# Kernel optimization log

Measured on AMD Instinct MI355X. Metric: run time of the kernel, lower is better.

Reference implementation:

```python
import jax, jax.numpy as jnp
import numpy as np

N, E, F_IN, H, C, P, E2, B, NCLS = 150000, 1500000, 64, 64, 50000, 300000, 600000, 16, 10
EPS = 1e-5


def setup_inputs() -> dict:
    key = jax.random.key(0)
    ks = jax.random.split(key, 20)
    f32 = jnp.float32

    def lin_w(k, i, o):
        return jax.random.normal(k, (i, o), f32) / np.float32(np.sqrt(i))

    return {
        "x": jax.random.normal(ks[0], (N, F_IN), f32),
        "edge_index": jax.random.randint(ks[1], (2, E), 0, N),
        "weights": jax.random.uniform(ks[2], (E,), f32),
        "batch": jnp.sort(jax.random.randint(ks[3], (N,), 0, B)),
        "cover_n": jax.random.randint(ks[4], (P,), 0, N),
        "cover_c": jax.random.randint(ks[5], (P,), 0, C),
        "edge_index2": jax.random.randint(ks[6], (2, E2), 0, C),
        "weights2": jax.random.uniform(ks[7], (E2,), f32),
        "batch2": jnp.sort(jax.random.randint(ks[8], (C,), 0, B)),
        "W_in0": lin_w(ks[9], F_IN, H), "b_in0": jnp.zeros((H,), f32),
        "W_in1": lin_w(ks[10], H, H), "b_in1": jnp.zeros((H,), f32),
        "Wl_in": lin_w(ks[11], 2 * H, H), "bl_in": jnp.zeros((H,), f32),
        "W_b0": lin_w(ks[12], 2 * H, H), "b_b0": jnp.zeros((H,), f32),
        "W_b1": lin_w(ks[13], H, H), "b_b1": jnp.zeros((H,), f32),
        "Wl_b": lin_w(ks[14], 2 * H, H), "bl_b": jnp.zeros((H,), f32),
        "bn_gamma": jnp.ones((4 * H,), f32), "bn_beta": jnp.zeros((4 * H,), f32),
        "lin1_W": lin_w(ks[15], 4 * H, H), "lin1_b": jnp.zeros((H,), f32),
        "lin2_W": lin_w(ks[16], H, NCLS), "lin2_b": jnp.zeros((NCLS,), f32),
    }


def _gcn(x, row, col, ew, W, b, n):
    # GCNConv with edge weights: sym-normalized adjacency, messages flow row->col
    h = x @ W
    deg = jax.ops.segment_sum(ew, col, num_segments=n)
    dis = jnp.where(deg > 0, jax.lax.rsqrt(deg), 0.0)
    norm = dis[row] * ew * dis[col]  # [E']
    return jax.ops.segment_sum(norm[:, None] * h[row], col, num_segments=n) + b


def _block(x, edge_index, ew, n, W0, b0, W1, b1, Wl, bl):
    # Block(num_layers=2, mode='cat'): two GCN+relu, JK-cat, Linear
    loop = jnp.arange(n)
    row = jnp.concatenate([edge_index[0], loop])  # add self loops (w=1)
    col = jnp.concatenate([edge_index[1], loop])
    ew = jnp.concatenate([ew, jnp.ones((n,), ew.dtype)])
    x1 = jax.nn.relu(_gcn(x, row, col, ew, W0, b0, n))
    x2 = jax.nn.relu(_gcn(x1, row, col, ew, W1, b1, n))
    return jnp.concatenate([x1, x2], axis=1) @ Wl + bl


def _segmax0(x, ids, n):
    m = jax.ops.segment_max(x, ids, num_segments=n)
    return jnp.where(jnp.isfinite(m), m, 0.0)  # empty segments -> 0


def reference(x, edge_index, weights, batch, cover_n, cover_c, edge_index2,
              weights2, batch2, W_in0, b_in0, W_in1, b_in1, Wl_in, bl_in,
              W_b0, b_b0, W_b1, b_b1, Wl_b, bl_b, bn_gamma, bn_beta,
              lin1_W, lin1_b, lin2_W, lin2_b):
    # conv_in on the original graph
    x1 = jax.nn.relu(_block(x, edge_index, weights, N,
                            W_in0, b_in0, W_in1, b_in1, Wl_in, bl_in))
    xs = [jax.ops.segment_sum(x1, batch, num_segments=B), _segmax0(x1, batch, B)]
    # cover-index scatter pooling: add + max over clusters
    xg = x1[cover_n]  # [P, H]
    xp = jnp.concatenate([
        jax.ops.segment_sum(xg, cover_c, num_segments=C),
        _segmax0(xg, cover_c, C),
    ], axis=1)  # [C, 2H]
    # block on the pooled graph
    x2 = jax.nn.relu(_block(xp, edge_index2, weights2, C,
                            W_b0, b_b0, W_b1, b_b1, Wl_b, bl_b))
    xs += [jax.ops.segment_sum(x2, batch2, num_segments=B), _segmax0(x2, batch2, B)]
    h = jnp.concatenate(xs, axis=1)  # [B, 4H]
    mu = h.mean(axis=0)
    var = ((h - mu) ** 2).mean(axis=0)
    h = (h - mu) * jax.lax.rsqrt(var + EPS) * bn_gamma + bn_beta
    h = jax.nn.relu(h @ lin1_W + lin1_b)
    return jax.nn.softmax(h @ lin2_W + lin2_b, axis=-1)
```

## Files before the change

### kernel.cpp

```cpp
#include <hip/hip_runtime.h>

#define N_NODES 150000
#define E_EDGES 1500000
#define C_CLUST 50000
#define P_PAIRS 300000
#define E2_EDGES 600000
#define B_BATCH 16
#define EPS_ 1e-5f

static __device__ __forceinline__ void atomicMaxFloatPos(float* addr, float v) {
    atomicMax((int*)addr, __float_as_int(v));
}


__global__ void cnt_ids_kernel(const int* __restrict__ ids, int* __restrict__ cnt, int P) {
    int p = blockIdx.x * blockDim.x + threadIdx.x;
    if (p < P) atomicAdd(&cnt[ids[p]], 1);
}

__global__ __launch_bounds__(256) void scan1_kernel(const int* __restrict__ cnt,
                                                    int* __restrict__ exc,
                                                    int* __restrict__ bsum, int n) {
    __shared__ int sh[256];
    int t = threadIdx.x;
    int base = blockIdx.x * 1024 + t * 4;
    int v[4];
    #pragma unroll
    for (int i = 0; i < 4; ++i) { int idx = base + i; v[i] = (idx < n) ? cnt[idx] : 0; }
    int tsum = v[0] + v[1] + v[2] + v[3];
    sh[t] = tsum; __syncthreads();
    for (int o = 1; o < 256; o <<= 1) {
        int add = (t >= o) ? sh[t - o] : 0;
        __syncthreads();
        sh[t] += add;
        __syncthreads();
    }
    int run = sh[t] - tsum;
    #pragma unroll
    for (int i = 0; i < 4; ++i) { int idx = base + i; if (idx < n) exc[idx] = run; run += v[i]; }
    if (t == 255) bsum[blockIdx.x] = sh[255];
}

__global__ __launch_bounds__(256) void scan2_kernel(int* __restrict__ bsum, int nb,
                                                    int* __restrict__ total_out) {
    __shared__ int sh[256];
    int t = threadIdx.x;
    int val = (t < nb) ? bsum[t] : 0;
    sh[t] = val; __syncthreads();
    for (int o = 1; o < 256; o <<= 1) {
        int add = (t >= o) ? sh[t - o] : 0;
        __syncthreads();
        sh[t] += add;
        __syncthreads();
    }
    if (t < nb) bsum[t] = sh[t] - val;
    if (t == nb - 1) *total_out = sh[t];
}

__global__ void scan3_kernel(const int* __restrict__ exc, const int* __restrict__ bsum,
                             int* __restrict__ rowptr, int* __restrict__ next, int n) {
    int i = blockIdx.x * blockDim.x + threadIdx.x;
    if (i < n) {
        int v = exc[i] + bsum[i >> 10];
        rowptr[i] = v;
        next[i] = v;
    }
}


__global__ void bucket_kernel(const int* __restrict__ ei, const float* __restrict__ ew,
                              int* __restrict__ next, int* __restrict__ src,
                              float* __restrict__ ewc, int E) {
    int e = blockIdx.x * blockDim.x + threadIdx.x;
    if (e >= E) return;
    int r = ei[e], c = ei[E + e];
    int pos = atomicAdd(&next[c], 1);
    src[pos] = r;
    ewc[pos] = ew[e];
}

__global__ void bucketP_kernel(const int* __restrict__ cn, const int* __restrict__ cc,
                               int* __restrict__ next, int* __restrict__ srcn, int P) {
    int p = blockIdx.x * blockDim.x + threadIdx.x;
    if (p >= P) return;
    int pos = atomicAdd(&next[cc[p]], 1);
    srcn[pos] = cn[p];
}


__global__ void dis_csr_kernel(const int* __restrict__ rowptr, const float* __restrict__ ewc,
                               float* __restrict__ dis, int n) {
    int c = blockIdx.x * blockDim.x + threadIdx.x;
    if (c >= n) return;
    int j0 = rowptr[c], j1 = rowptr[c + 1];
    float s = 0.f;
    for (int j = j0; j < j1; ++j) s += ewc[j];
    dis[c] = rsqrtf(s + 1.0f);
}


__global__ void nw_csr_kernel(const int* __restrict__ rowptr, const int* __restrict__ src,
                              float* __restrict__ ewc, const float* __restrict__ dis, int n) {
    int c = blockIdx.x * blockDim.x + threadIdx.x;
    if (c >= n) return;
    float dc = dis[c];
    int j0 = rowptr[c], j1 = rowptr[c + 1];
    for (int j = j0; j < j1; ++j)
        ewc[j] = dis[src[j]] * ewc[j] * dc;
}


__global__ void gcn_gather_kernel(const float* __restrict__ h, const int* __restrict__ rowptr,
                                  const int* __restrict__ src, const float* __restrict__ nw,
                                  const float* __restrict__ dis, const float* __restrict__ bias,
                                  float* __restrict__ out, int n) {
    int t = blockIdx.x * blockDim.x + threadIdx.x;
    int c = t >> 6, lane = t & 63;
    if (c >= n) return;
    float d = dis[c];
    float acc = bias[lane] + d * d * h[(size_t)c * 64 + lane];
    int j = rowptr[c], e1 = rowptr[c + 1];
    for (; j + 3 < e1; j += 4) {
        int   r0 = src[j],  r1 = src[j + 1], r2 = src[j + 2], r3 = src[j + 3];
        float w0 = nw[j],   w1 = nw[j + 1],  w2 = nw[j + 2],  w3 = nw[j + 3];
        float h0 = h[(size_t)r0 * 64 + lane];
        float h1 = h[(size_t)r1 * 64 + lane];
        float h2 = h[(size_t)r2 * 64 + lane];
        float h3 = h[(size_t)r3 * 64 + lane];
        acc += w0 * h0; acc += w1 * h1; acc += w2 * h2; acc += w3 * h3;
    }
    for (; j < e1; ++j) acc += nw[j] * h[(size_t)src[j] * 64 + lane];
    out[(size_t)c * 64 + lane] = acc;
}

__global__ void cover_gather_kernel(const float* __restrict__ X, const int* __restrict__ rowptr,
                                    const int* __restrict__ srcn, float* __restrict__ xp_sum,
                                    float* __restrict__ xp_max, int C) {
    int t = blockIdx.x * blockDim.x + threadIdx.x;
    int c = t >> 6, lane = t & 63;
    if (c >= C) return;
    float s = 0.f, m = 0.f;
    int j = rowptr[c], e1 = rowptr[c + 1];
    for (; j + 1 < e1; j += 2) {
        float v0 = X[(size_t)srcn[j] * 64 + lane];
        float v1 = X[(size_t)srcn[j + 1] * 64 + lane];
        s += v0 + v1; m = fmaxf(m, fmaxf(v0, v1));
    }
    if (j < e1) {
        float v = X[(size_t)srcn[j] * 64 + lane];
        s += v; m = fmaxf(m, v);
    }
    xp_sum[(size_t)c * 64 + lane] = s;
    xp_max[(size_t)c * 64 + lane] = m;
}


template<int K, bool RELU_IN, bool RELU_OUT, bool HAS_X2, bool HAS_BIAS>
__global__ __launch_bounds__(256) void gemm_kernel(const float* __restrict__ X1,
                                                   const float* __restrict__ X2,
                                                   const float* __restrict__ W,
                                                   const float* __restrict__ bias,
                                                   float* __restrict__ Y, int n) {
    constexpr int KP = K + 4;
    __shared__ float Xs[64 * KP];
    __shared__ float Ws[K * 64];
    const int tid = threadIdx.x;
    const int r0 = blockIdx.x * 64;

    for (int i = tid; i < K * 16; i += 256)
        ((float4*)Ws)[i] = ((const float4*)W)[i];

    for (int i = tid; i < 16 * K; i += 256) {
        int row = i / (K / 4);
        int k4  = (i % (K / 4)) * 4;
        int r = r0 + row;
        float4 v = make_float4(0.f, 0.f, 0.f, 0.f);
        if (r < n) {
            const float* s = (HAS_X2 && k4 >= 64) ? (X2 + (size_t)r * 64 + (k4 - 64))
                                                  : (X1 + (size_t)r * 64 + k4);
            v = *(const float4*)s;
            if (RELU_IN) {
                v.x = fmaxf(v.x, 0.f); v.y = fmaxf(v.y, 0.f);
                v.z = fmaxf(v.z, 0.f); v.w = fmaxf(v.w, 0.f);
            }
        }
        *(float4*)&Xs[row * KP + k4] = v;
    }
    __syncthreads();

    const int tx = tid & 15, ty = tid >> 4;
    const int c0 = tx * 4, rl = ty * 4;
    float acc[4][4] = {};

    for (int k = 0; k < K; k += 4) {
        float4 xv[4], wv[4];
        #pragma unroll
        for (int i = 0; i < 4; ++i) xv[i] = *(const float4*)&Xs[(rl + i) * KP + k];
        #pragma unroll
        for (int i = 0; i < 4; ++i) wv[i] = *(const float4*)&Ws[(k + i) * 64 + c0];
        #pragma unroll
        for (int i = 0; i < 4; ++i) {
            const float* xp = (const float*)&xv[i];
            #pragma unroll
            for (int kk = 0; kk < 4; ++kk) {
                const float* wp = (const float*)&wv[kk];
                #pragma unroll
                for (int j = 0; j < 4; ++j) acc[i][j] += xp[kk] * wp[j];
            }
        }
    }

    #pragma unroll
    for (int i = 0; i < 4; ++i) {
        int r = r0 + rl + i;
        if (r < n) {
            float o[4];
            #pragma unroll
            for (int j = 0; j < 4; ++j) {
                o[j] = acc[i][j];
                if (HAS_BIAS) o[j] += bias[c0 + j];
                if (RELU_OUT) o[j] = fmaxf(o[j], 0.f);
            }
            *(float4*)&Y[(size_t)r * 64 + c0] = make_float4(o[0], o[1], o[2], o[3]);
        }
    }
}


__global__ void batch_pool_kernel(const float* __restrict__ X, const int* __restrict__ batch,
                                  int n, float* __restrict__ xs, int col_off, int rows_per_block) {
    int lane = threadIdx.x;
    int rstart = blockIdx.x * rows_per_block;
    if (rstart >= n) return;
    int rend = min(rstart + rows_per_block, n);
    float s = 0.f, m = 0.f;
    int cur = batch[rstart];
    for (int r = rstart; r < rend; ++r) {
        int b = batch[r];
        if (b != cur) {
            atomicAdd(&xs[cur * 256 + col_off + lane], s);
            atomicMaxFloatPos(&xs[cur * 256 + col_off + 64 + lane], m);
            s = 0.f; m = 0.f; cur = b;
        }
        float v = X[(size_t)r * 64 + lane];
        s += v; m = fmaxf(m, v);
    }
    atomicAdd(&xs[cur * 256 + col_off + lane], s);
    atomicMaxFloatPos(&xs[cur * 256 + col_off + 64 + lane], m);
}


__global__ __launch_bounds__(256) void head_kernel(const float* __restrict__ xs,
    const float* __restrict__ gamma, const float* __restrict__ beta,
    const float* __restrict__ W1, const float* __restrict__ b1,
    const float* __restrict__ W2, const float* __restrict__ b2,
    float* __restrict__ out) {
    __shared__ float hn[16][256];
    __shared__ float h2[16][64];
    __shared__ float logits[16][10];
    int t = threadIdx.x;

    float v[16];
    float mu = 0.f;
    #pragma unroll
    for (int b = 0; b < 16; ++b) { v[b] = xs[b * 256 + t]; mu += v[b]; }
    mu *= (1.f / 16.f);
    float var = 0.f;
    #pragma unroll
    for (int b = 0; b < 16; ++b) { float d = v[b] - mu; var += d * d; }
    var *= (1.f / 16.f);
    float sc = rsqrtf(var + EPS_) * gamma[t];
    float bt = beta[t];
    #pragma unroll
    for (int b = 0; b < 16; ++b) hn[b][t] = (v[b] - mu) * sc + bt;
    __syncthreads();

    {
        int c = t & 63, bg = t >> 6;
        for (int j = 0; j < 4; ++j) {
            int b = bg * 4 + j;
            float acc = b1[c];
            for (int k = 0; k < 256; ++k) acc += hn[b][k] * W1[k * 64 + c];
            h2[b][c] = fmaxf(acc, 0.f);
        }
    }
    __syncthreads();

    if (t < 160) {
        int b = t / 10, c = t % 10;
        float acc = b2[c];
        for (int k = 0; k < 64; ++k) acc += h2[b][k] * W2[k * 10 + c];
        logits[b][c] = acc;
    }
    __syncthreads();

    if (t < 16) {
        float m = -1e30f;
        for (int c = 0; c < 10; ++c) m = fmaxf(m, logits[t][c]);
        float s = 0.f;
        float e[10];
        for (int c = 0; c < 10; ++c) { e[c] = expf(logits[t][c] - m); s += e[c]; }
        float inv = 1.f / s;
        for (int c = 0; c < 10; ++c) out[t * 10 + c] = e[c] * inv;
    }
}

extern "C" void kernel_launch(void* const* d_in, const int* in_sizes, int n_in,
                              void* d_out, int out_size, void* d_ws, size_t ws_size,
                              hipStream_t stream) {
    (void)in_sizes; (void)n_in; (void)out_size; (void)ws_size;
    const float* x      = (const float*)d_in[0];
    const int*   ei1    = (const int*)d_in[1];
    const float* w1     = (const float*)d_in[2];
    const int*   batch  = (const int*)d_in[3];
    const int*   covern = (const int*)d_in[4];
    const int*   coverc = (const int*)d_in[5];
    const int*   ei2    = (const int*)d_in[6];
    const float* w2     = (const float*)d_in[7];
    const int*   batch2 = (const int*)d_in[8];
    const float* W_in0  = (const float*)d_in[9];
    const float* b_in0  = (const float*)d_in[10];
    const float* W_in1  = (const float*)d_in[11];
    const float* b_in1  = (const float*)d_in[12];
    const float* Wl_in  = (const float*)d_in[13];
    const float* bl_in  = (const float*)d_in[14];
    const float* W_b0   = (const float*)d_in[15];
    const float* b_b0   = (const float*)d_in[16];
    const float* W_b1   = (const float*)d_in[17];
    const float* b_b1   = (const float*)d_in[18];
    const float* Wl_b   = (const float*)d_in[19];
    const float* bl_b   = (const float*)d_in[20];
    const float* gamma  = (const float*)d_in[21];
    const float* beta   = (const float*)d_in[22];
    const float* lin1W  = (const float*)d_in[23];
    const float* lin1b  = (const float*)d_in[24];
    const float* lin2W  = (const float*)d_in[25];
    const float* lin2b  = (const float*)d_in[26];
    float* out = (float*)d_out;

    char* ws = (char*)d_ws;
    size_t off = 0;
    auto alloc = [&](size_t bytes) {
        char* p = ws + off; off += (bytes + 255) & ~(size_t)255; return p;
    };
    float* A   = (float*)alloc((size_t)N_NODES * 64 * 4);
    float* Bb  = (float*)alloc((size_t)N_NODES * 64 * 4);
    float* Cc  = (float*)alloc((size_t)N_NODES * 64 * 4);
    float* D   = (float*)alloc((size_t)N_NODES * 4);
    float* XS  = (float*)alloc((size_t)B_BATCH * 256 * 4);
    int*   bsum = (int*)alloc(256 * 4);
    char*  csr  = alloc(14 * 1024 * 1024);

    int*   cnt1    = (int*)csr;
    int*   next1   = cnt1 + N_NODES;
    int*   rowptr1 = next1 + N_NODES;
    int*   src1    = rowptr1 + (N_NODES + 1);
    float* nw1     = (float*)(src1 + E_EDGES);
    int*   cnt2    = (int*)csr;
    int*   next2   = cnt2 + C_CLUST;
    int*   rowptr2 = next2 + C_CLUST;
    int*   src2    = rowptr2 + (C_CLUST + 1);
    float* nw2     = (float*)(src2 + E2_EDGES);
    int*   cntP    = (int*)(nw2 + E2_EDGES);
    int*   nextP   = cntP + C_CLUST;
    int*   rowptrP = nextP + C_CLUST;
    int*   srcP    = rowptrP + (C_CLUST + 1);

    float* A2     = A  + (size_t)C_CLUST * 64;
    float* xp_sum = Bb;
    float* xp_max = Bb + (size_t)C_CLUST * 64;

    auto cdiv = [](long long a, long long b) { return (int)((a + b - 1) / b); };

    hipMemsetAsync(XS, 0, B_BATCH * 256 * 4, stream);

    hipMemsetAsync(cnt1, 0, N_NODES * 4, stream);
    cnt_ids_kernel<<<cdiv(E_EDGES, 256), 256, 0, stream>>>(ei1 + E_EDGES, cnt1, E_EDGES);
    scan1_kernel<<<cdiv(N_NODES, 1024), 256, 0, stream>>>(cnt1, next1, bsum, N_NODES);
    scan2_kernel<<<1, 256, 0, stream>>>(bsum, cdiv(N_NODES, 1024), rowptr1 + N_NODES);
    scan3_kernel<<<cdiv(N_NODES, 256), 256, 0, stream>>>(next1, bsum, rowptr1, next1, N_NODES);
    bucket_kernel<<<cdiv(E_EDGES, 256), 256, 0, stream>>>(ei1, w1, next1, src1, nw1, E_EDGES);
    dis_csr_kernel<<<cdiv(N_NODES, 256), 256, 0, stream>>>(rowptr1, nw1, D, N_NODES);
    nw_csr_kernel<<<cdiv(N_NODES, 256), 256, 0, stream>>>(rowptr1, src1, nw1, D, N_NODES);

    gemm_kernel<64, false, false, false, false><<<cdiv(N_NODES, 64), 256, 0, stream>>>(
        x, nullptr, W_in0, nullptr, A, N_NODES);
    gcn_gather_kernel<<<cdiv((long long)N_NODES * 64, 256), 256, 0, stream>>>(
        A, rowptr1, src1, nw1, D, b_in0, Bb, N_NODES);
    gemm_kernel<64, true, false, false, false><<<cdiv(N_NODES, 64), 256, 0, stream>>>(
        Bb, nullptr, W_in1, nullptr, A, N_NODES);
    gcn_gather_kernel<<<cdiv((long long)N_NODES * 64, 256), 256, 0, stream>>>(
        A, rowptr1, src1, nw1, D, b_in1, Cc, N_NODES);
    gemm_kernel<128, true, true, true, true><<<cdiv(N_NODES, 64), 256, 0, stream>>>(
        Bb, Cc, Wl_in, bl_in, A, N_NODES);

    batch_pool_kernel<<<cdiv(N_NODES, 64), 64, 0, stream>>>(A, batch, N_NODES, XS, 0, 64);

    hipMemsetAsync(cntP, 0, C_CLUST * 4, stream);
    cnt_ids_kernel<<<cdiv(P_PAIRS, 256), 256, 0, stream>>>(coverc, cntP, P_PAIRS);
    scan1_kernel<<<cdiv(C_CLUST, 1024), 256, 0, stream>>>(cntP, nextP, bsum, C_CLUST);
    scan2_kernel<<<1, 256, 0, stream>>>(bsum, cdiv(C_CLUST, 1024), rowptrP + C_CLUST);
    scan3_kernel<<<cdiv(C_CLUST, 256), 256, 0, stream>>>(nextP, bsum, rowptrP, nextP, C_CLUST);
    bucketP_kernel<<<cdiv(P_PAIRS, 256), 256, 0, stream>>>(covern, coverc, nextP, srcP, P_PAIRS);
    cover_gather_kernel<<<cdiv((long long)C_CLUST * 64, 256), 256, 0, stream>>>(
        A, rowptrP, srcP, xp_sum, xp_max, C_CLUST);

    hipMemsetAsync(cnt2, 0, C_CLUST * 4, stream);
    cnt_ids_kernel<<<cdiv(E2_EDGES, 256), 256, 0, stream>>>(ei2 + E2_EDGES, cnt2, E2_EDGES);
    scan1_kernel<<<cdiv(C_CLUST, 1024), 256, 0, stream>>>(cnt2, next2, bsum, C_CLUST);
    scan2_kernel<<<1, 256, 0, stream>>>(bsum, cdiv(C_CLUST, 1024), rowptr2 + C_CLUST);
    scan3_kernel<<<cdiv(C_CLUST, 256), 256, 0, stream>>>(next2, bsum, rowptr2, next2, C_CLUST);
    bucket_kernel<<<cdiv(E2_EDGES, 256), 256, 0, stream>>>(ei2, w2, next2, src2, nw2, E2_EDGES);
    dis_csr_kernel<<<cdiv(C_CLUST, 256), 256, 0, stream>>>(rowptr2, nw2, D, C_CLUST);
    nw_csr_kernel<<<cdiv(C_CLUST, 256), 256, 0, stream>>>(rowptr2, src2, nw2, D, C_CLUST);

    gemm_kernel<128, false, false, true, false><<<cdiv(C_CLUST, 64), 256, 0, stream>>>(
        xp_sum, xp_max, W_b0, nullptr, Cc, C_CLUST);
    gcn_gather_kernel<<<cdiv((long long)C_CLUST * 64, 256), 256, 0, stream>>>(
        Cc, rowptr2, src2, nw2, D, b_b0, A, C_CLUST);
    gemm_kernel<64, true, false, false, false><<<cdiv(C_CLUST, 64), 256, 0, stream>>>(
        A, nullptr, W_b1, nullptr, Cc, C_CLUST);
    gcn_gather_kernel<<<cdiv((long long)C_CLUST * 64, 256), 256, 0, stream>>>(
        Cc, rowptr2, src2, nw2, D, b_b1, A2, C_CLUST);
    gemm_kernel<128, true, true, true, true><<<cdiv(C_CLUST, 64), 256, 0, stream>>>(
        A, A2, Wl_b, bl_b, Cc, C_CLUST);

    batch_pool_kernel<<<cdiv(C_CLUST, 64), 64, 0, stream>>>(Cc, batch2, C_CLUST, XS, 128, 64);

    head_kernel<<<1, 256, 0, stream>>>(XS, gamma, beta, lin1W, lin1b, lin2W, lin2b, out);
}
```

Baseline: 927.7 us.

## Fuse GCN gather with following dense linear layers via wave shuffles

Replaces the separate gather, gemm, gather and JK-concat gemm kernels with a fused kernel. Each wavefront aggregates neighbours for a node and immediately multiplies the relu'd result by a weight matrix staged in shared memory, using lane shuffles. This removes intermediate activation round-trips through global memory and several launches. The cost is a per-node 64- or 128-step shuffle matvec and a weight reload into shared memory for every block of 16 nodes.

```diff
diff --git a/kernel.cpp b/kernel.cpp
--- a/kernel.cpp
+++ b/kernel.cpp
@@ -109,28 +109,60 @@
         ewc[j] = dis[src[j]] * ewc[j] * dc;
 }
 
-
-__global__ void gcn_gather_kernel(const float* __restrict__ h, const int* __restrict__ rowptr,
-                                  const int* __restrict__ src, const float* __restrict__ nw,
-                                  const float* __restrict__ dis, const float* __restrict__ bias,
-                                  float* __restrict__ out, int n) {
-    int t = blockIdx.x * blockDim.x + threadIdx.x;
-    int c = t >> 6, lane = t & 63;
-    if (c >= n) return;
-    float d = dis[c];
-    float acc = bias[lane] + d * d * h[(size_t)c * 64 + lane];
-    int j = rowptr[c], e1 = rowptr[c + 1];
-    for (; j + 3 < e1; j += 4) {
-        int   r0 = src[j],  r1 = src[j + 1], r2 = src[j + 2], r3 = src[j + 3];
-        float w0 = nw[j],   w1 = nw[j + 1],  w2 = nw[j + 2],  w3 = nw[j + 3];
-        float h0 = h[(size_t)r0 * 64 + lane];
-        float h1 = h[(size_t)r1 * 64 + lane];
-        float h2 = h[(size_t)r2 * 64 + lane];
-        float h3 = h[(size_t)r3 * 64 + lane];
-        acc += w0 * h0; acc += w1 * h1; acc += w2 * h2; acc += w3 * h3;
-    }
-    for (; j < e1; ++j) acc += nw[j] * h[(size_t)src[j] * 64 + lane];
-    out[(size_t)c * 64 + lane] = acc;
+template<bool HAS_PRE>
+__global__ __launch_bounds__(256) void fused_gather_gemm_kernel(
+    const float* __restrict__ h, const int* __restrict__ rowptr,
+    const int* __restrict__ src, const float* __restrict__ nw,
+    const float* __restrict__ dis, const float* __restrict__ bias_g,
+    const float* __restrict__ pre, const float* __restrict__ W,
+    const float* __restrict__ bias2, float* __restrict__ agg_out,
+    float* __restrict__ out, int n) {
+    constexpr int KW = HAS_PRE ? 128 : 64;
+    __shared__ float Ws[KW * 64];
+    const int tid = threadIdx.x;
+    for (int i = tid; i < KW * 16; i += 256)
+        ((float4*)Ws)[i] = ((const float4*)W)[i];
+    __syncthreads();
+
+    const int lane = tid & 63, wid = tid >> 6;
+    const int c0 = blockIdx.x * 16 + wid * 4;
+    for (int i = 0; i < 4; ++i) {
+        int c = c0 + i;
+        if (c >= n) break;
+        float d = dis[c];
+        float acc = bias_g[lane] + d * d * h[(size_t)c * 64 + lane];
+        int j = rowptr[c], e1 = rowptr[c + 1];
+        for (; j + 3 < e1; j += 4) {
+            int   r0 = src[j],  r1 = src[j + 1], r2 = src[j + 2], r3 = src[j + 3];
+            float w0 = nw[j],   w1 = nw[j + 1],  w2 = nw[j + 2],  w3 = nw[j + 3];
+            acc += w0 * h[(size_t)r0 * 64 + lane];
+            acc += w1 * h[(size_t)r1 * 64 + lane];
+            acc += w2 * h[(size_t)r2 * 64 + lane];
+            acc += w3 * h[(size_t)r3 * 64 + lane];
+        }
+        for (; j < e1; ++j) acc += nw[j] * h[(size_t)src[j] * 64 + lane];
+
+        if (agg_out) agg_out[(size_t)c * 64 + lane] = acc;
+        float r2v = fmaxf(acc, 0.f);
+
+        float acc2 = 0.f;
+        if (HAS_PRE) {
+            float r1v = fmaxf(pre[(size_t)c * 64 + lane], 0.f);
+            #pragma unroll
+            for (int k = 0; k < 64; ++k)
+                acc2 += __shfl(r1v, k) * Ws[k * 64 + lane];
+            #pragma unroll
+            for (int k = 0; k < 64; ++k)
+                acc2 += __shfl(r2v, k) * Ws[(64 + k) * 64 + lane];
+            acc2 += bias2[lane];
+            acc2 = fmaxf(acc2, 0.f);
+        } else {
+            #pragma unroll
+            for (int k = 0; k < 64; ++k)
+                acc2 += __shfl(r2v, k) * Ws[k * 64 + lane];
+        }
+        out[(size_t)c * 64 + lane] = acc2;
+    }
 }
 
 __global__ void cover_gather_kernel(const float* __restrict__ X, const int* __restrict__ rowptr,
@@ -385,14 +417,10 @@
 
     gemm_kernel<64, false, false, false, false><<<cdiv(N_NODES, 64), 256, 0, stream>>>(
         x, nullptr, W_in0, nullptr, A, N_NODES);
-    gcn_gather_kernel<<<cdiv((long long)N_NODES * 64, 256), 256, 0, stream>>>(
-        A, rowptr1, src1, nw1, D, b_in0, Bb, N_NODES);
-    gemm_kernel<64, true, false, false, false><<<cdiv(N_NODES, 64), 256, 0, stream>>>(
-        Bb, nullptr, W_in1, nullptr, A, N_NODES);
-    gcn_gather_kernel<<<cdiv((long long)N_NODES * 64, 256), 256, 0, stream>>>(
-        A, rowptr1, src1, nw1, D, b_in1, Cc, N_NODES);
-    gemm_kernel<128, true, true, true, true><<<cdiv(N_NODES, 64), 256, 0, stream>>>(
-        Bb, Cc, Wl_in, bl_in, A, N_NODES);
+    fused_gather_gemm_kernel<false><<<cdiv(N_NODES, 16), 256, 0, stream>>>(
+        A, rowptr1, src1, nw1, D, b_in0, nullptr, W_in1, nullptr, Bb, Cc, N_NODES);
+    fused_gather_gemm_kernel<true><<<cdiv(N_NODES, 16), 256, 0, stream>>>(
+        Cc, rowptr1, src1, nw1, D, b_in1, Bb, Wl_in, bl_in, nullptr, A, N_NODES);
 
     batch_pool_kernel<<<cdiv(N_NODES, 64), 64, 0, stream>>>(A, batch, N_NODES, XS, 0, 64);
 
@@ -416,16 +444,12 @@
 
     gemm_kernel<128, false, false, true, false><<<cdiv(C_CLUST, 64), 256, 0, stream>>>(
         xp_sum, xp_max, W_b0, nullptr, Cc, C_CLUST);
-    gcn_gather_kernel<<<cdiv((long long)C_CLUST * 64, 256), 256, 0, stream>>>(
-        Cc, rowptr2, src2, nw2, D, b_b0, A, C_CLUST);
-    gemm_kernel<64, true, false, false, false><<<cdiv(C_CLUST, 64), 256, 0, stream>>>(
-        A, nullptr, W_b1, nullptr, Cc, C_CLUST);
-    gcn_gather_kernel<<<cdiv((long long)C_CLUST * 64, 256), 256, 0, stream>>>(
-        Cc, rowptr2, src2, nw2, D, b_b1, A2, C_CLUST);
-    gemm_kernel<128, true, true, true, true><<<cdiv(C_CLUST, 64), 256, 0, stream>>>(
-        A, A2, Wl_b, bl_b, Cc, C_CLUST);
-
-    batch_pool_kernel<<<cdiv(C_CLUST, 64), 64, 0, stream>>>(Cc, batch2, C_CLUST, XS, 128, 64);
+    fused_gather_gemm_kernel<false><<<cdiv(C_CLUST, 16), 256, 0, stream>>>(
+        Cc, rowptr2, src2, nw2, D, b_b0, nullptr, W_b1, nullptr, Bb, A, C_CLUST);
+    fused_gather_gemm_kernel<true><<<cdiv(C_CLUST, 16), 256, 0, stream>>>(
+        A, rowptr2, src2, nw2, D, b_b1, Bb, Wl_b, bl_b, nullptr, A2, C_CLUST);
+
+    batch_pool_kernel<<<cdiv(C_CLUST, 64), 64, 0, stream>>>(A2, batch2, C_CLUST, XS, 128, 64);
 
     head_kernel<<<1, 256, 0, stream>>>(XS, gamma, beta, lin1W, lin1b, lin2W, lin2b, out);
 }
```

Result: slower. 1.183 ms (+27.5%).
